# Optimization experiments

Hardware: AMD Instinct MI355X
Metric: run time of the kernel (lower is better)

The kernel has to match this reference:

```python
import jax, jax.numpy as jnp
import numpy as np

N, E = 50000, 600000
DIN, D, C = 239, 128, 2
NEG_SLOPE_MLP = 0.01   # nn.LeakyReLU default
NEG_SLOPE_ATT = 0.2    # GATConv default


def leaky(x, s):
    return jnp.where(x >= 0, x, s * x)


def setup_inputs() -> dict:
    key = jax.random.key(0)
    ks = jax.random.split(key, 12)
    sc = lambda d: 1.0 / np.sqrt(d)
    return {
        "x": jax.random.normal(ks[0], (N, DIN), jnp.float32),
        "edge_index": jax.random.randint(ks[1], (2, E), 0, N, jnp.int32),
        "edge_type": jax.random.randint(ks[2], (E,), 0, 4, jnp.int32),
        "W_in": jax.random.normal(ks[3], (DIN, D), jnp.float32) * sc(DIN),
        "b_in": jnp.zeros((D,), jnp.float32),
        "W_gat": jax.random.normal(ks[4], (D, D), jnp.float32) * sc(D),
        "att_src": jax.random.normal(ks[5], (D,), jnp.float32) * sc(D),
        "att_dst": jax.random.normal(ks[6], (D,), jnp.float32) * sc(D),
        "b_gat": jnp.zeros((D,), jnp.float32),
        "W_h": jax.random.normal(ks[7], (D, D), jnp.float32) * sc(D),
        "b_h": jnp.zeros((D,), jnp.float32),
        "W_out": jax.random.normal(ks[8], (D, C), jnp.float32) * sc(D),
        "b_out": jnp.zeros((C,), jnp.float32),
    }


def reference(x, edge_index, edge_type, W_in, b_in, W_gat, att_src, att_dst,
              b_gat, W_h, b_h, W_out, b_out):
    # input encoder: Linear + LeakyReLU
    h = leaky(x @ W_in + b_in, NEG_SLOPE_MLP)                      # [N, D]

    # GATConv (heads=1): add self loops, edge attention, segment softmax over dst
    loops = jnp.arange(N, dtype=edge_index.dtype)
    src = jnp.concatenate([edge_index[0], loops])                  # [E+N]
    dst = jnp.concatenate([edge_index[1], loops])

    g = h @ W_gat                                                  # [N, D]
    a_src = g @ att_src                                            # [N]
    a_dst = g @ att_dst                                            # [N]
    e = leaky(a_src[src] + a_dst[dst], NEG_SLOPE_ATT)              # [E+N]

    m = jax.ops.segment_max(e, dst, num_segments=N)                # self-loops => no empty segs
    w = jnp.exp(e - m[dst])
    z = jax.ops.segment_sum(w, dst, num_segments=N)
    alpha = w / z[dst]                                             # [E+N]

    out = jax.ops.segment_sum(alpha[:, None] * g[src], dst, num_segments=N) + b_gat

    # dropout is identity in eval mode
    h2 = leaky(out @ W_h + b_h, NEG_SLOPE_MLP)
    return h2 @ W_out + b_out                                      # [N, C]
```

## Files before the change

### kernel.cpp

```cpp
#include <hip/hip_runtime.h>

#define NNODE 50000
#define NEDGE 600000
#define KDIN  239
#define DDIM  128
#define NTILES 3125
#define NBG   782
#define NBUCK 256
#define BSZ   196
#define HBSZ  98
#define NPB   128
#define CHP   4688
#define ESCAP 4096

typedef _Float16 half8 __attribute__((ext_vector_type(8)));
typedef _Float16 half4 __attribute__((ext_vector_type(4)));
typedef __attribute__((ext_vector_type(4))) float f32x4;

__device__ __forceinline__ ushort f2h(float f){
  union { _Float16 h; ushort u; } c; c.h = (_Float16)f; return c.u;
}

__global__ __launch_bounds__(256) void pre_k(
    const float* __restrict__ W_in, const float* __restrict__ W_gat, const float* __restrict__ W_h,
    ushort* __restrict__ BfA, ushort* __restrict__ BfB, ushort* __restrict__ BfC,
    const int* __restrict__ ei, int* __restrict__ cpart)
{
  __shared__ int hb[NBUCK];
  const int b = blockIdx.x, t = threadIdx.x;
  if (b < NPB){
    hb[t] = 0;
    __syncthreads();
    const int e0 = b*CHP, e1 = min(NEDGE, e0+CHP);
    for (int e=e0+t; e<e1; e+=256){
      int dst = min(max(ei[NEDGE+e],0), NNODE-1);
      atomicAdd(&hb[dst/BSZ], 1);
    }
    __syncthreads();
    cpart[b*NBUCK + t] = hb[t];
  } else if (b < NPB + 128){
    int idx = (b-NPB)*256 + t; int n = idx >> 8, k = idx & 255;
    BfA[idx] = (k < KDIN) ? f2h(W_in[(size_t)k*DDIM + n]) : (ushort)0;
  } else if (b < NPB + 192){
    int idx = (b-NPB-128)*256 + t; int n = idx >> 7, k = idx & 127;
    BfB[idx] = f2h(W_gat[(size_t)k*DDIM + n]);
  } else {
    int idx = (b-NPB-192)*256 + t; int n = idx >> 7, k = idx & 127;
    BfC[idx] = f2h(W_h[(size_t)k*DDIM + n]);
  }
}

__global__ __launch_bounds__(256, 3) void gemmAB_k(
    const float* __restrict__ x, const ushort* __restrict__ BfA,
    const ushort* __restrict__ BfB, const float* __restrict__ b_in,
    ushort* __restrict__ gf,
    const float* __restrict__ vs, const float* __restrict__ vd,
    float* __restrict__ os, float* __restrict__ od,
    float* __restrict__ bms, float* __restrict__ bmd,
    const int* __restrict__ ei, const int* __restrict__ cpart, int* __restrict__ pairs,
    int* __restrict__ gmS)
{
  __shared__ __attribute__((aligned(16))) ushort Bs[128*128];
  __shared__ __attribute__((aligned(16))) ushort ht[4][16*128];
  if (blockIdx.x < NPB){
    int* cur = (int*)Bs;
    int* scn = ((int*)Bs) + NBUCK;
    const int pb = blockIdx.x, t = threadIdx.x;
    int tot = 0, before = 0;
    #pragma unroll 8
    for (int i=0;i<NPB;i++){
      const int c = cpart[i*NBUCK + t];
      if (i < pb) before += c;
      tot += c;
    }
    scn[t] = tot;
    __syncthreads();
    #pragma unroll
    for (int off=1; off<NBUCK; off<<=1){
      int v = (t>=off) ? scn[t-off] : 0;
      __syncthreads();
      scn[t] += v;
      __syncthreads();
    }
    const int S = scn[t] - tot;
    cur[t] = S + before;
    if (pb == 0) gmS[t] = S;
    __syncthreads();
    const int e0 = pb*CHP, e1 = min(NEDGE, e0+CHP);
    for (int e=e0+t; e<e1; e+=256){
      int dst = min(max(ei[NEDGE+e],0), NNODE-1);
      int src = min(max(ei[e],0), NNODE-1);
      int bk = (unsigned)dst / BSZ;
      int pos = atomicAdd(&cur[bk], 1);
      pairs[pos] = src | ((dst - bk*BSZ) << 16);
    }
    return;
  }
  const int lane = threadIdx.x & 63;
  const int wave = threadIdx.x >> 6;
  const int q = lane >> 4, c = lane & 15;
  const int tile = (blockIdx.x - NPB)*4 + wave;
  const bool act = tile < NTILES;
  const int rowBase = tile*16;
  const int swz = (c&7)<<4;
  f32x4 acc[8];
  half8 af[8];
  if (act){
    const float* __restrict__ ap = x + (size_t)(rowBase + c)*KDIN;
    #pragma unroll
    for (int s=0;s<7;s++){
      const float* __restrict__ p = ap + s*32 + q*8;
      #pragma unroll
      for (int i=0;i<8;i++) af[s][i] = (_Float16)p[i];
    }
    #pragma unroll
    for (int i=0;i<8;i++){
      const int k = 224 + q*8 + i;
      af[7][i] = (_Float16)((k < KDIN) ? ap[k] : 0.f);
    }
    #pragma unroll
    for (int t=0;t<8;t++) acc[t] = (f32x4){0.f,0.f,0.f,0.f};
  }
  #pragma unroll
  for (int H=0; H<2; ++H){
    #pragma unroll
    for (int it=0; it<8; ++it){
      const int idx = it*256 + threadIdx.x;
      const int row = idx >> 4, sl = (idx & 15)*16;
      const half8 v = *(const half8*)(BfA + (size_t)row*256 + H*128 + (idx & 15)*8);
      *(half8*)((char*)Bs + row*256 + (sl ^ ((row&7)<<4))) = v;
    }
    __syncthreads();
    if (act){
      const char* __restrict__ bsl = (const char*)Bs + c*256;
      #pragma unroll
      for (int s=0;s<4;s++){
        const int so = (s*64 + q*16) ^ swz;
        #pragma unroll
        for (int t=0;t<8;t++){
          const half8 bf = *(const half8*)(bsl + t*16*256 + so);
          acc[t] = __builtin_amdgcn_mfma_f32_16x16x32_f16(af[H*4+s], bf, acc[t], 0,0,0);
        }
      }
    }
    __syncthreads();
  }
  if (act){
    char* __restrict__ hw = (char*)&ht[wave][0];
    #pragma unroll
    for (int t=0;t<8;t++){
      const int col = 16*t + c;
      const float bv = b_in[col];
      #pragma unroll
      for (int r=0;r<4;r++){
        const int row = q*4 + r;
        float v = acc[t][r] + bv;
        v = (v >= 0.f) ? v : 0.01f*v;
        *(_Float16*)(hw + ((row*256 + col*2) ^ ((row&7)<<4))) = (_Float16)v;
      }
    }
  }
  #pragma unroll
  for (int it=0; it<8; ++it){
    const int idx = it*256 + threadIdx.x;
    const int row = idx >> 4, sl = (idx & 15)*16;
    const half8 v = *(const half8*)(BfB + (size_t)idx*8);
    *(half8*)((char*)Bs + row*256 + (sl ^ ((row&7)<<4))) = v;
  }
  __syncthreads();
  if (!act) return;
  half8 af2[4];
  const char* __restrict__ hr = (const char*)&ht[wave][0] + c*256;
  #pragma unroll
  for (int s=0;s<4;s++) af2[s] = *(const half8*)(hr + ((s*64 + q*16) ^ swz));
  #pragma unroll
  for (int t=0;t<8;t++) acc[t] = (f32x4){0.f,0.f,0.f,0.f};
  const char* __restrict__ bsl2 = (const char*)Bs + c*256;
  #pragma unroll
  for (int s=0;s<4;s++){
    const int so = (s*64 + q*16) ^ swz;
    #pragma unroll
    for (int t=0;t<8;t++){
      const half8 bf = *(const half8*)(bsl2 + t*16*256 + so);
      acc[t] = __builtin_amdgcn_mfma_f32_16x16x32_f16(af2[s], bf, acc[t], 0,0,0);
    }
  }
  float pr0[4] = {0,0,0,0}, pr1[4] = {0,0,0,0};
  #pragma unroll
  for (int t=0;t<8;t++){
    const int col = 16*t + c;
    const float va = vs[col], vb = vd[col];
    #pragma unroll
    for (int r=0;r<4;r++){
      const int row = rowBase + q*4 + r;
      const float v = acc[t][r];
      gf[(size_t)row*DDIM + col] = f2h(v);
      pr0[r] += v*va; pr1[r] += v*vb;
    }
  }
  float lmax_s = -3.0e38f, lmax_d = -3.0e38f;
  #pragma unroll
  for (int r=0;r<4;r++){
    float s0 = pr0[r], s1 = pr1[r];
    s0 += __shfl_xor(s0,8); s1 += __shfl_xor(s1,8);
    s0 += __shfl_xor(s0,4); s1 += __shfl_xor(s1,4);
    s0 += __shfl_xor(s0,2); s1 += __shfl_xor(s1,2);
    s0 += __shfl_xor(s0,1); s1 += __shfl_xor(s1,1);
    lmax_s = fmaxf(lmax_s, s0); lmax_d = fmaxf(lmax_d, s1);
    if (c == 0){
      const int row = rowBase + q*4 + r;
      os[row] = s0; od[row] = s1;
    }
  }
  #pragma unroll
  for (int off=32; off>0; off>>=1){
    lmax_s = fmaxf(lmax_s, __shfl_xor(lmax_s, off));
    lmax_d = fmaxf(lmax_d, __shfl_xor(lmax_d, off));
  }
  if (lane == 0){ bms[tile] = lmax_s; bmd[tile] = lmax_d; }
}

__global__ __launch_bounds__(1024, 2) void fineagg_k(
    const int* __restrict__ pairs, const int* __restrict__ gmS,
    int* __restrict__ es, const ushort* __restrict__ gf,
    const float* __restrict__ a_src, const float* __restrict__ a_dst,
    const float* __restrict__ bms, const float* __restrict__ bmd,
    const float* __restrict__ b_gat, ushort* __restrict__ og)
{
  __shared__ int fh[256];
  __shared__ int sc2[256];
  __shared__ int offL[256];
  __shared__ int degL[256];
  __shared__ int esL[ESCAP];
  __shared__ float Msh;
  const int b = blockIdx.x >> 1;
  const int hf2 = blockIdx.x & 1;
  const int t = threadIdx.x;
  float ms = -3.0e38f, md = -3.0e38f;
  for (int i=t; i<NTILES; i+=1024){ ms = fmaxf(ms, bms[i]); md = fmaxf(md, bmd[i]); }
  #pragma unroll
  for (int off=32; off>0; off>>=1){
    ms = fmaxf(ms, __shfl_xor(ms, off));
    md = fmaxf(md, __shfl_xor(md, off));
  }
  float* red = (float*)sc2;
  const int w = t >> 6;
  if ((t & 63) == 0){ red[w] = ms; red[16+w] = md; }
  __syncthreads();
  if (t == 0){
    float As = red[0], Ad = red[16];
    #pragma unroll
    for (int i=1;i<16;i++){ As = fmaxf(As, red[i]); Ad = fmaxf(Ad, red[16+i]); }
    float M = As + Ad;
    Msh = (M >= 0.f) ? M : 0.2f*M;
  }
  if (t < 256) fh[t] = 0;
  __syncthreads();
  const int s0 = gmS[b];
  const int s1 = (b < NBUCK-1) ? gmS[b+1] : NEDGE;
  const bool fit = (s1 - s0) <= ESCAP;
  for (int i=s0+t; i<s1; i+=1024)
    atomicAdd(&fh[pairs[i] >> 16], 1);
  __syncthreads();
  int deg = 0;
  if (t < 256){ deg = fh[t]; sc2[t] = deg; }
  __syncthreads();
  #pragma unroll
  for (int off=1; off<256; off<<=1){
    int v = (t < 256 && t >= off) ? sc2[t-off] : 0;
    __syncthreads();
    if (t < 256) sc2[t] += v;
    __syncthreads();
  }
  if (t < 256){
    const int excl = sc2[t] - deg;
    offL[t] = excl;
    degL[t] = deg;
    fh[t] = excl;
  }
  __syncthreads();
  for (int i=s0+t; i<s1; i+=1024){
    const int p = pairs[i];
    const int pos = atomicAdd(&fh[p >> 16], 1);
    if (fit) esL[pos] = p & 0xFFFF;
    else if (hf2 == 0) es[s0 + pos] = p & 0xFFFF;
  }
  __syncthreads();
  const float M = Msh;
  const int lane = t & 63;
  const int half = lane >> 5, li = lane & 31;
  const int slot = (t >> 6)*2 + half;
  const int D0 = hf2*HBSZ, D1 = hf2 ? BSZ : HBSZ;
  const float4 bg = *(const float4*)&b_gat[li*4];
  for (int d = D0 + slot; d < D1; d += 32){
    const int dst = b*BSZ + d;
    if (dst >= NNODE) continue;
    const float ad = a_dst[dst];
    f32x4 a0={0,0,0,0}, a1={0,0,0,0}, a2={0,0,0,0}, a3={0,0,0,0};
    float w0s=0.f, w1s=0.f, w2s=0.f, w3s=0.f;
    if (fit){
      const int start = offL[d];
      const int dg = degL[d];
      const int* __restrict__ bin = esL + start;
      int j = 0;
      for (; j+3 < dg; j += 4){
        const int i0=bin[j], i1=bin[j+1], i2=bin[j+2], i3=bin[j+3];
        float e0=a_src[i0]+ad; e0=(e0>=0.f)?e0:0.2f*e0;
        float e1=a_src[i1]+ad; e1=(e1>=0.f)?e1:0.2f*e1;
        float e2=a_src[i2]+ad; e2=(e2>=0.f)?e2:0.2f*e2;
        float e3=a_src[i3]+ad; e3=(e3>=0.f)?e3:0.2f*e3;
        const float w0=__expf(e0-M), w1=__expf(e1-M), w2=__expf(e2-M), w3=__expf(e3-M);
        const half4 g0 = *(const half4*)(gf + (size_t)i0*DDIM + li*4);
        const half4 g1 = *(const half4*)(gf + (size_t)i1*DDIM + li*4);
        const half4 g2 = *(const half4*)(gf + (size_t)i2*DDIM + li*4);
        const half4 g3 = *(const half4*)(gf + (size_t)i3*DDIM + li*4);
        #pragma unroll
        for (int i=0;i<4;i++){
          a0[i] += w0*(float)g0[i]; a1[i] += w1*(float)g1[i];
          a2[i] += w2*(float)g2[i]; a3[i] += w3*(float)g3[i];
        }
        w0s += w0; w1s += w1; w2s += w2; w3s += w3;
      }
      for (; j < dg; ++j){
        const int si = bin[j];
        float e0=a_src[si]+ad; e0=(e0>=0.f)?e0:0.2f*e0;
        const float w2v = __expf(e0-M);
        const half4 gv = *(const half4*)(gf + (size_t)si*DDIM + li*4);
        #pragma unroll
        for (int i=0;i<4;i++) a0[i] += w2v*(float)gv[i];
        w0s += w2v;
      }
    } else {
      for (int i=s0; i<s1; ++i){
        const int p = pairs[i];
        if ((p >> 16) != d) continue;
        const int si = p & 0xFFFF;
        float e0=a_src[si]+ad; e0=(e0>=0.f)?e0:0.2f*e0;
        const float w2v = __expf(e0-M);
        const half4 gv = *(const half4*)(gf + (size_t)si*DDIM + li*4);
        #pragma unroll
        for (int i2v=0;i2v<4;i2v++) a0[i2v] += w2v*(float)gv[i2v];
        w0s += w2v;
      }
    }
    {
      float evs=a_src[dst]+ad; evs=(evs>=0.f)?evs:0.2f*evs;
      const float w2v = __expf(evs-M);
      const half4 gv = *(const half4*)(gf + (size_t)dst*DDIM + li*4);
      #pragma unroll
      for (int i=0;i<4;i++) a0[i] += w2v*(float)gv[i];
      w0s += w2v;
    }
    const float inv = 1.f/(w0s+w1s+w2s+w3s);
    ushort4 o;
    o.x = f2h((a0[0]+a1[0]+a2[0]+a3[0])*inv + bg.x);
    o.y = f2h((a0[1]+a1[1]+a2[1]+a3[1])*inv + bg.y);
    o.z = f2h((a0[2]+a1[2]+a2[2]+a3[2])*inv + bg.z);
    o.w = f2h((a0[3]+a1[3]+a2[3]+a3[3])*inv + bg.w);
    *(ushort4*)(og + (size_t)dst*DDIM + li*4) = o;
  }
}

__global__ __launch_bounds__(256, 4) void gemmC_k(
    const ushort* __restrict__ Af, const ushort* __restrict__ Btf,
    const float* __restrict__ bias, float* __restrict__ outf,
    const float* __restrict__ Wo, const float* __restrict__ bo)
{
  constexpr int Kpad = 128, Kb = 256;
  __shared__ __attribute__((aligned(16))) ushort Bs[128*Kpad];
  #pragma unroll
  for (int it=0; it<8; ++it){
    const int idx = it*256 + threadIdx.x;
    const int row = idx >> 4, sl = (idx & 15)*16;
    const half8 v = *(const half8*)(Btf + (size_t)idx*8);
    *(half8*)((char*)Bs + row*Kb + (sl ^ ((row&7)<<4))) = v;
  }
  __syncthreads();
  const int lane = threadIdx.x & 63;
  const int wave = threadIdx.x >> 6;
  const int q = lane >> 4, c = lane & 15;
  const int tile = blockIdx.x*4 + wave;
  if (tile >= NTILES) return;
  const int rowBase = tile*16;
  half8 af[4];
  const ushort* __restrict__ ap = Af + (size_t)(rowBase + c)*Kpad + q*8;
  #pragma unroll
  for (int s=0;s<4;s++) af[s] = *(const half8*)(ap + s*32);
  f32x4 acc[8];
  #pragma unroll
  for (int t=0;t<8;t++) acc[t] = (f32x4){0.f,0.f,0.f,0.f};
  const int swz = (c&7)<<4;
  const char* __restrict__ bsl = (const char*)Bs + c*Kb;
  #pragma unroll
  for (int s=0;s<4;s++){
    const int so = (s*64 + q*16) ^ swz;
    #pragma unroll
    for (int t=0;t<8;t++){
      const half8 bf = *(const half8*)(bsl + t*16*Kb + so);
      acc[t] = __builtin_amdgcn_mfma_f32_16x16x32_f16(af[s], bf, acc[t], 0,0,0);
    }
  }
  float pr0[4] = {0,0,0,0}, pr1[4] = {0,0,0,0};
  #pragma unroll
  for (int t=0;t<8;t++){
    const int col = 16*t + c;
    const float bv = bias[col];
    const float va = Wo[2*col], vb = Wo[2*col+1];
    #pragma unroll
    for (int r=0;r<4;r++){
      float v = acc[t][r] + bv;
      v = (v >= 0.f) ? v : 0.01f*v;
      pr0[r] += v*va; pr1[r] += v*vb;
    }
  }
  #pragma unroll
  for (int r=0;r<4;r++){
    float s0 = pr0[r], s1 = pr1[r];
    s0 += __shfl_xor(s0,8); s1 += __shfl_xor(s1,8);
    s0 += __shfl_xor(s0,4); s1 += __shfl_xor(s1,4);
    s0 += __shfl_xor(s0,2); s1 += __shfl_xor(s1,2);
    s0 += __shfl_xor(s0,1); s1 += __shfl_xor(s1,1);
    if (c == 0){
      const int row = rowBase + q*4 + r;
      float2 y2; y2.x = s0 + bo[0]; y2.y = s1 + bo[1];
      *(float2*)&outf[(size_t)row*2] = y2;
    }
  }
}

extern "C" void kernel_launch(void* const* d_in, const int* in_sizes, int n_in,
                              void* d_out, int out_size, void* d_ws, size_t ws_size,
                              hipStream_t stream)
{
  const float* x       = (const float*)d_in[0];
  const int*   ei      = (const int*)d_in[1];
  const float* W_in    = (const float*)d_in[3];
  const float* b_in    = (const float*)d_in[4];
  const float* W_gat   = (const float*)d_in[5];
  const float* att_src = (const float*)d_in[6];
  const float* att_dst = (const float*)d_in[7];
  const float* b_gat   = (const float*)d_in[8];
  const float* W_h     = (const float*)d_in[9];
  const float* b_h     = (const float*)d_in[10];
  const float* W_out   = (const float*)d_in[11];
  const float* b_out   = (const float*)d_in[12];

  char* ws = (char*)d_ws;
  ushort*   gf     = (ushort*)  (ws + 0);
  ushort*   og     = (ushort*)  (ws + 12800000);
  ushort*   BfA    = (ushort*)  (ws + 25600000);
  ushort*   BfB    = (ushort*)  (ws + 25800000);
  ushort*   BfC    = (ushort*)  (ws + 25900000);
  int*      cpart  = (int*)     (ws + 26000000);
  int*      pairs  = (int*)     (ws + 26300000);
  int*      es     = (int*)     (ws + 28700000);
  float*    a_src  = (float*)   (ws + 31100000);
  float*    a_dst  = (float*)   (ws + 31300000);
  int*      gmS    = (int*)     (ws + 31500000);
  float*    bmaxS  = (float*)   (ws + 31600000);
  float*    bmaxD  = (float*)   (ws + 31616000);

  pre_k<<<NPB + 256, 256, 0, stream>>>(W_in, W_gat, W_h, BfA, BfB, BfC, ei, cpart);
  gemmAB_k<<<NPB + NBG, 256, 0, stream>>>(x, BfA, BfB, b_in, gf,
      att_src, att_dst, a_src, a_dst, bmaxS, bmaxD, ei, cpart, pairs, gmS);
  fineagg_k<<<2*NBUCK, 1024, 0, stream>>>(pairs, gmS, es, gf, a_src, a_dst,
      bmaxS, bmaxD, b_gat, og);
  gemmC_k<<<NBG, 256, 0, stream>>>(og, BfC, b_h, (float*)d_out, W_out, b_out);
}
```

Measured before the change: 168.0 us.

## Give each wave a private 8KB LDS weight slab and drop block barriers in fused GEMM

The fused input-encoder and GAT-projection GEMM kernel no longer stages full 128x128 weight tiles in a block-shared buffer guarded by __syncthreads. Each wave now streams 64x64 weight sub-tiles into its own 8KB LDS region and reuses that region to hold the hidden activations. This cuts LDS per block from roughly 48KB to 32KB, raises the occupancy hint from 3 to 4 blocks per CU, and removes cross-wave barriers so idle tail waves can exit early. In exchange, each wave redundantly loads the full weights from global/L2 (4x more weight traffic per block), and the same-wave LDS reuse relies on wave-synchronous ordering without explicit barriers.

```diff
diff --git a/kernel.cpp b/kernel.cpp
--- a/kernel.cpp
+++ b/kernel.cpp
@@ -50,7 +50,7 @@
   }
 }
 
-__global__ __launch_bounds__(256, 3) void gemmAB_k(
+__global__ __launch_bounds__(256, 4) void gemmAB_k(
     const float* __restrict__ x, const ushort* __restrict__ BfA,
     const ushort* __restrict__ BfB, const float* __restrict__ b_in,
     ushort* __restrict__ gf,
@@ -60,8 +60,7 @@
     const int* __restrict__ ei, const int* __restrict__ cpart, int* __restrict__ pairs,
     int* __restrict__ gmS)
 {
-  __shared__ __attribute__((aligned(16))) ushort Bs[128*128];
-  __shared__ __attribute__((aligned(16))) ushort ht[4][16*128];
+  __shared__ __attribute__((aligned(16))) ushort Bs[4*4096];
   if (blockIdx.x < NPB){
     int* cur = (int*)Bs;
     int* scn = ((int*)Bs) + NBUCK;
@@ -100,12 +99,12 @@
   const int wave = threadIdx.x >> 6;
   const int q = lane >> 4, c = lane & 15;
   const int tile = (blockIdx.x - NPB)*4 + wave;
-  const bool act = tile < NTILES;
+  if (tile >= NTILES) return;
   const int rowBase = tile*16;
   const int swz = (c&7)<<4;
-  f32x4 acc[8];
+  char* bw = (char*)Bs + wave*8192;
   half8 af[8];
-  if (act){
+  {
     const float* __restrict__ ap = x + (size_t)(rowBase + c)*KDIN;
     #pragma unroll
     for (int s=0;s<7;s++){
@@ -118,71 +117,69 @@
       const int k = 224 + q*8 + i;
       af[7][i] = (_Float16)((k < KDIN) ? ap[k] : 0.f);
     }
-    #pragma unroll
-    for (int t=0;t<8;t++) acc[t] = (f32x4){0.f,0.f,0.f,0.f};
-  }
-  #pragma unroll
-  for (int H=0; H<2; ++H){
-    #pragma unroll
-    for (int it=0; it<8; ++it){
-      const int idx = it*256 + threadIdx.x;
-      const int row = idx >> 4, sl = (idx & 15)*16;
-      const half8 v = *(const half8*)(BfA + (size_t)row*256 + H*128 + (idx & 15)*8);
-      *(half8*)((char*)Bs + row*256 + (sl ^ ((row&7)<<4))) = v;
-    }
-    __syncthreads();
-    if (act){
-      const char* __restrict__ bsl = (const char*)Bs + c*256;
-      #pragma unroll
-      for (int s=0;s<4;s++){
-        const int so = (s*64 + q*16) ^ swz;
+  }
+  f32x4 acc[8];
+  #pragma unroll
+  for (int t=0;t<8;t++) acc[t] = (f32x4){0.f,0.f,0.f,0.f};
+  #pragma unroll
+  for (int s2=0; s2<4; ++s2){
+    #pragma unroll
+    for (int h=0; h<2; ++h){
+      #pragma unroll
+      for (int i=0;i<8;++i){
+        const int j = i*64 + lane;
+        const int nl = j>>3, kc = j&7;
+        const half8 v = *(const half8*)(BfA + (size_t)(h*64+nl)*256 + s2*64 + kc*8);
+        *(half8*)(bw + nl*128 + ((kc*16) ^ ((nl&7)<<4))) = v;
+      }
+      #pragma unroll
+      for (int sp=0; sp<2; ++sp){
         #pragma unroll
-        for (int t=0;t<8;t++){
-          const half8 bf = *(const half8*)(bsl + t*16*256 + so);
-          acc[t] = __builtin_amdgcn_mfma_f32_16x16x32_f16(af[H*4+s], bf, acc[t], 0,0,0);
+        for (int t=0;t<4;++t){
+          const int rl = 16*t + c;
+          const half8 bf = *(const half8*)(bw + rl*128 + ((sp*64 + q*16) ^ swz));
+          acc[h*4+t] = __builtin_amdgcn_mfma_f32_16x16x32_f16(af[s2*2+sp], bf, acc[h*4+t], 0,0,0);
         }
       }
     }
-    __syncthreads();
-  }
-  if (act){
-    char* __restrict__ hw = (char*)&ht[wave][0];
-    #pragma unroll
-    for (int t=0;t<8;t++){
-      const int col = 16*t + c;
-      const float bv = b_in[col];
-      #pragma unroll
-      for (int r=0;r<4;r++){
-        const int row = q*4 + r;
-        float v = acc[t][r] + bv;
-        v = (v >= 0.f) ? v : 0.01f*v;
-        *(_Float16*)(hw + ((row*256 + col*2) ^ ((row&7)<<4))) = (_Float16)v;
-      }
-    }
-  }
-  #pragma unroll
-  for (int it=0; it<8; ++it){
-    const int idx = it*256 + threadIdx.x;
-    const int row = idx >> 4, sl = (idx & 15)*16;
-    const half8 v = *(const half8*)(BfB + (size_t)idx*8);
-    *(half8*)((char*)Bs + row*256 + (sl ^ ((row&7)<<4))) = v;
-  }
-  __syncthreads();
-  if (!act) return;
+  }
+  #pragma unroll
+  for (int t=0;t<8;t++){
+    const int col = 16*t + c;
+    const float bv = b_in[col];
+    #pragma unroll
+    for (int r=0;r<4;r++){
+      const int row = q*4 + r;
+      float v = acc[t][r] + bv;
+      v = (v >= 0.f) ? v : 0.01f*v;
+      *(_Float16*)(bw + ((row*256 + col*2) ^ ((row&7)<<4))) = (_Float16)v;
+    }
+  }
   half8 af2[4];
-  const char* __restrict__ hr = (const char*)&ht[wave][0] + c*256;
-  #pragma unroll
-  for (int s=0;s<4;s++) af2[s] = *(const half8*)(hr + ((s*64 + q*16) ^ swz));
+  #pragma unroll
+  for (int s=0;s<4;s++) af2[s] = *(const half8*)(bw + c*256 + ((s*64 + q*16) ^ swz));
   #pragma unroll
   for (int t=0;t<8;t++) acc[t] = (f32x4){0.f,0.f,0.f,0.f};
-  const char* __restrict__ bsl2 = (const char*)Bs + c*256;
-  #pragma unroll
-  for (int s=0;s<4;s++){
-    const int so = (s*64 + q*16) ^ swz;
-    #pragma unroll
-    for (int t=0;t<8;t++){
-      const half8 bf = *(const half8*)(bsl2 + t*16*256 + so);
-      acc[t] = __builtin_amdgcn_mfma_f32_16x16x32_f16(af2[s], bf, acc[t], 0,0,0);
+  #pragma unroll
+  for (int h2=0; h2<2; ++h2){
+    #pragma unroll
+    for (int k2=0; k2<2; ++k2){
+      #pragma unroll
+      for (int i=0;i<8;++i){
+        const int j = i*64 + lane;
+        const int nl = j>>3, kc = j&7;
+        const half8 v = *(const half8*)(BfB + (size_t)(h2*64+nl)*128 + k2*64 + kc*8);
+        *(half8*)(bw + nl*128 + ((kc*16) ^ ((nl&7)<<4))) = v;
+      }
+      #pragma unroll
+      for (int sp=0; sp<2; ++sp){
+        #pragma unroll
+        for (int t=0;t<4;++t){
+          const int rl = 16*t + c;
+          const half8 bf = *(const half8*)(bw + rl*128 + ((sp*64 + q*16) ^ swz));
+          acc[h2*4+t] = __builtin_amdgcn_mfma_f32_16x16x32_f16(af2[k2*2+sp], bf, acc[h2*4+t], 0,0,0);
+        }
+      }
     }
   }
   float pr0[4] = {0,0,0,0}, pr1[4] = {0,0,0,0};
```

Result: slower. 181.3 us (+8.0%).
